# Kernel optimization log

Measured on AMD Instinct MI355X. Metric: run time of the kernel, lower is better.

## Reference

```python
import jax, jax.numpy as jnp
import numpy as np

DIM = 512
HEADS = 8
R = 28          # resolution2 (query grid); input spatial = 2*R
B = 4
GN_GROUPS = 32
GN_EPS = 1e-5


def _conv(x, w, stride=1, pad=0, groups=1):
    return jax.lax.conv_general_dilated(
        x, w, (stride, stride), [(pad, pad), (pad, pad)],
        dimension_numbers=('NCHW', 'OIHW', 'NCHW'), feature_group_count=groups)


def _gn(x, w, b, groups=GN_GROUPS, eps=GN_EPS):
    Bn, C, H, W = x.shape
    xg = x.reshape(Bn, groups, C // groups, H, W)
    m = xg.mean(axis=(2, 3, 4), keepdims=True)
    v = xg.var(axis=(2, 3, 4), keepdims=True)
    xg = (xg - m) * jax.lax.rsqrt(v + eps)
    return xg.reshape(Bn, C, H, W) * w[None, :, None, None] + b[None, :, None, None]


def _l2norm_axis1(x, eps=1e-12):
    # torch F.normalize default: dim=1 (here: the heads axis), clamp_min on norm
    n = jnp.sqrt(jnp.sum(x * x, axis=1, keepdims=True))
    return x / jnp.maximum(n, eps)


def _hardswish(x):
    return x * jnp.clip(x + 3.0, 0.0, 6.0) * (1.0 / 6.0)


def _bias_idxs(r):
    # offset (|2*i1-i2|, |2*j1-j2|) -> unique id oy*(2r)+ox; table [r*r, (2r)*(2r)]
    oy = np.abs(2 * np.arange(r)[:, None] - np.arange(2 * r)[None, :])  # [r, 2r]
    ox = oy
    idx = oy[:, None, :, None] * (2 * r) + ox[None, :, None, :]  # [r, r, 2r, 2r]
    return jnp.asarray(idx.reshape(r * r, 4 * r * r), dtype=jnp.int32)


def setup_inputs() -> dict:
    key = jax.random.key(0)
    ks = jax.random.split(key, 16)
    dim, heads, r = DIM, HEADS, R
    cin = dim // 2
    H = 2 * r
    rn = lambda k, s, sc: jax.random.normal(k, s, jnp.float32) * sc
    ones = lambda s: jnp.ones(s, jnp.float32)
    zeros = lambda s: jnp.zeros(s, jnp.float32)
    return {
        'x': rn(ks[0], (B, cin, H, H), 1.0),
        'q_local_w': rn(ks[1], (cin, 1, 3, 3), 0.1),
        'q_local_b': zeros((cin,)),
        'q_proj_w': rn(ks[2], (dim, cin, 1, 1), 0.05),
        'q_proj_b': zeros((dim,)),
        'q_gn_w': ones((dim,)), 'q_gn_b': zeros((dim,)),
        'k_w': rn(ks[3], (dim, cin, 1, 1), 0.05),
        'k_gn_w': ones((dim,)), 'k_gn_b': zeros((dim,)),
        'v_w': rn(ks[4], (dim, cin, 1, 1), 0.05),
        'v_gn_w': ones((dim,)), 'v_gn_b': zeros((dim,)),
        'loc_w': rn(ks[5], (dim, dim // heads, 3, 3), 0.05),
        'loc_b': zeros((dim,)),
        'loc_gn_w': ones((dim,)), 'loc_gn_b': zeros((dim,)),
        'th1_w': rn(ks[6], (heads, heads), 0.3),
        'th2_w': rn(ks[7], (heads, heads), 0.3),
        'out_w': rn(ks[8], (dim, dim, 1, 1), 0.05),
        'out_gn_w': ones((dim,)), 'out_gn_b': zeros((dim,)),
        'proj_w': rn(ks[9], (dim, cin, 3, 3), 0.05),
        'proj_b': zeros((dim,)),
        'proj_gn_w': ones((dim,)), 'proj_gn_b': zeros((dim,)),
        'attn_biases': rn(ks[10], (heads, (2 * r) * (2 * r)), 0.02),
        'bias_idxs': _bias_idxs(r),
    }


def reference(x, q_local_w, q_local_b, q_proj_w, q_proj_b, q_gn_w, q_gn_b,
              k_w, k_gn_w, k_gn_b, v_w, v_gn_w, v_gn_b,
              loc_w, loc_b, loc_gn_w, loc_gn_b, th1_w, th2_w,
              out_w, out_gn_w, out_gn_b, proj_w, proj_b, proj_gn_w, proj_gn_b,
              attn_biases, bias_idxs):
    Bn, cin, H, W = x.shape
    dim, heads = DIM, HEADS
    hd = dim // heads
    N = H * W
    r = H // 2
    N2 = r * r
    scale = hd ** -0.5

    # residual projection branch: 3x3 s2 conv + GN
    x_proj = _gn(_conv(x, proj_w, 2, 1) + proj_b[None, :, None, None], proj_gn_w, proj_gn_b)

    # query downsampling: depthwise 3x3 s2 + stride-2 subsample (AvgPool k=1 s=2), then 1x1 + GN
    local_q = _conv(x, q_local_w, 2, 1, groups=cin) + q_local_b[None, :, None, None]
    pool_q = x[:, :, ::2, ::2]
    q = _gn(_conv(local_q + pool_q, q_proj_w) + q_proj_b[None, :, None, None], q_gn_w, q_gn_b)
    q = q.reshape(Bn, heads, hd, N2).transpose(0, 1, 3, 2)          # [B,h,N2,hd]

    k = _gn(_conv(x, k_w), k_gn_w, k_gn_b).reshape(Bn, heads, hd, N)  # [B,h,hd,N]

    v_map = _gn(_conv(x, v_w), v_gn_w, v_gn_b)                       # [B,dim,H,W]
    v_local = _gn(_conv(v_map, loc_w, 2, 1, groups=heads) + loc_b[None, :, None, None],
                  loc_gn_w, loc_gn_b)                                # [B,dim,r,r]
    v = v_map.reshape(Bn, heads, hd, N).transpose(0, 1, 3, 2)        # [B,h,N,hd]

    # cosine attention (normalized over heads axis, faithful to F.normalize dim=1)
    qn = _l2norm_axis1(q)
    kn = _l2norm_axis1(k)
    attn = jnp.einsum('bhqd,bhdn->bhqn', qn, kn) * scale \
        + attn_biases[:, bias_idxs][None]                            # [B,h,N2,N]

    # talking heads: 1x1 conv over heads axis, pre- and post-softmax
    attn = jnp.einsum('oi,biqn->boqn', th1_w, attn)
    attn = jax.nn.softmax(attn, axis=-1)
    attn = jnp.einsum('oi,biqn->boqn', th2_w, attn)

    out = jnp.einsum('bhqn,bhnd->bhqd', attn, v)                     # [B,h,N2,hd]
    out = out.transpose(0, 1, 3, 2).reshape(Bn, dim, r, r) + v_local
    out = _gn(_conv(_hardswish(out), out_w), out_gn_w, out_gn_b)
    return out + x_proj
```

## Files before the change

kernel.cpp:

```cpp
#include <hip/hip_runtime.h>
#include <stdint.h>

typedef unsigned short u16;
typedef unsigned int u32;
typedef __attribute__((ext_vector_type(8))) short bf16x8;
typedef __attribute__((ext_vector_type(4))) float f32x4;
typedef __attribute__((ext_vector_type(4))) u32 u32x4;

#define DEV static __device__ __forceinline__

DEV float bf2f(u16 v){ return __uint_as_float(((u32)v)<<16); }
DEV u16 f2bf(float f){
  u32 u = __float_as_uint(f);
  u32 r = (u + 0x7FFFu + ((u>>16)&1u)) >> 16;
  return (u16)r;
}
DEV float ldx(const void* p, long i, int f){
  return f ? ((const float*)p)[i] : bf2f(((const u16*)p)[i]);
}
DEV void unpk8(uint4 v, float* f){
  f[0]=__uint_as_float(v.x<<16); f[1]=__uint_as_float(v.x&0xFFFF0000u);
  f[2]=__uint_as_float(v.y<<16); f[3]=__uint_as_float(v.y&0xFFFF0000u);
  f[4]=__uint_as_float(v.z<<16); f[5]=__uint_as_float(v.z&0xFFFF0000u);
  f[6]=__uint_as_float(v.w<<16); f[7]=__uint_as_float(v.w&0xFFFF0000u);
}
DEV int iabs(int a){ return a<0? -a : a; }

__global__ void detect_k(const void* x, int* dflag){
  const u16* p = (const u16*)x;
  int t = threadIdx.x; int cnt = 0;
  for(int i=t;i<65536;i+=256){ int e=(p[i]>>7)&0xFF; if(e>=0xC0) cnt++; }
  __shared__ int r[256]; r[t]=cnt; __syncthreads();
  for(int o=128;o>0;o>>=1){ if(t<o) r[t]+=r[t+o]; __syncthreads(); }
  if(t==0) *dflag = (r[0] > 655) ? 1 : 0;
}
__global__ __launch_bounds__(256) void sanitize_k(void* o, long n, const int* df){
  int f = *df;
  long i = (long)blockIdx.x*256 + threadIdx.x;
  long st = (long)gridDim.x*256;
  if(f){
    float* p=(float*)o;
    for(; i<n; i+=st){ u32 u=__float_as_uint(p[i]); if((u&0x7F800000u)==0x7F800000u) p[i]=4096.f; }
  } else {
    u16* p=(u16*)o;
    u16 c = f2bf(4096.f);
    for(; i<n; i+=st){ if((p[i] & 0x7F80) == 0x7F80) p[i]=c; }
  }
}
__global__ void sentinel_k(u16* o, float v){ if(threadIdx.x==0) o[0] = f2bf(v); }
__global__ __launch_bounds__(256) void zero_k(float* __restrict__ p, long n){
  long i = (long)blockIdx.x*256 + threadIdx.x;
  long st = (long)gridDim.x*256;
  for(; i<n; i+=st) p[i]=0.f;
}

__global__ __launch_bounds__(256) void transp_k(const void* x, u16* __restrict__ xT, const int* df){
  __shared__ float T[32][33];
  int f = *df;
  int p0 = blockIdx.x*32, c0 = blockIdx.y*32, b = blockIdx.z;
  int tx = threadIdx.x & 31, ty = threadIdx.x >> 5;
  long base = (long)b*256*3136;
  #pragma unroll
  for(int i=0;i<4;i++){
    int c = c0 + ty + i*8;
    T[ty+i*8][tx] = ldx(x, base + (long)c*3136 + p0 + tx, f);
  }
  __syncthreads();
  #pragma unroll
  for(int i=0;i<4;i++){
    int p = p0 + ty + i*8;
    xT[((size_t)b*3136 + p)*256 + c0 + tx] = f2bf(T[tx][ty+i*8]);
  }
}

__global__ __launch_bounds__(256) void im2col_bt_k(const void* in, long bstride, u16* __restrict__ out,
                                                   int Cin, int isInput, const int* df){
  int f = isInput ? *df : 0;
  int K9 = Cin*9;
  int total = 784*K9;
  int id = blockIdx.x*256 + threadIdx.x;
  if(id>=total) return;
  long off = (long)blockIdx.y * bstride;
  u16* op = out + (size_t)blockIdx.y * total;
  int q = id / K9, r = id % K9;
  int ci = r/9, k = r%9;
  int oy=q/28, ox=q%28, ky=k/3, kx=k%3;
  int iy=2*oy-1+ky, ix=2*ox-1+kx;
  float v = 0.f;
  if((u32)iy<56u && (u32)ix<56u) v = ldx(in, off + (long)ci*3136 + iy*56+ix, f);
  op[id] = f2bf(v);
}

__global__ __launch_bounds__(256) void qlocal_bt_k(const void* x, const void* w,
                                                   const void* bias, u16* __restrict__ outT, const int* df){
  int f = *df;
  int id = blockIdx.x*256 + threadIdx.x;
  if(id >= 4*256*784) return;
  int q = id % 784; int r = id/784;
  int c = r % 256;  int b = r / 256;
  int oy = q/28, ox = q%28;
  long xp = (long)(b*256 + c)*3136;
  float acc = ldx(bias, c, f) + ldx(x, xp + (2*oy)*56 + 2*ox, f);
  #pragma unroll
  for(int ky=0;ky<3;ky++){
    int iy = 2*oy-1+ky;
    if((u32)iy>=56u) continue;
    #pragma unroll
    for(int kx=0;kx<3;kx++){
      int ix = 2*ox-1+kx;
      if((u32)ix>=56u) continue;
      acc += ldx(x, xp + iy*56+ix, f) * ldx(w, c*9+ky*3+kx, f);
    }
  }
  outT[((size_t)b*784 + q)*256 + c] = f2bf(acc);
}

__global__ __launch_bounds__(256) void hs_addT_k(const float* __restrict__ a, const u16* __restrict__ bsrc,
                                                 u16* __restrict__ outT){
  __shared__ float T[32][33];
  int q0 = blockIdx.x*32, c0 = blockIdx.y*32, b = blockIdx.z;
  int tx = threadIdx.x&31, ty = threadIdx.x>>5;
  #pragma unroll
  for(int i=0;i<4;i++){
    int c = c0+ty+i*8;
    int q = q0+tx;
    float s = 0.f;
    if(q < 784){
      size_t e = ((size_t)b*512 + c)*784 + q;
      s = a[e] + bf2f(bsrc[e]);
      float cl = fminf(fmaxf(s+3.f,0.f),6.f);
      s = s*cl*(1.f/6.f);
    }
    T[ty+i*8][tx] = s;
  }
  __syncthreads();
  #pragma unroll
  for(int i=0;i<4;i++){
    int q = q0+ty+i*8;
    if(q < 784) outT[((size_t)b*784 + q)*512 + c0+tx] = f2bf(T[tx][ty+i*8]);
  }
}

__global__ __launch_bounds__(256) void gemm_mfma_k(const void* A, const u16* __restrict__ BT,
                                                   void* C, const void* bias,
                                                   int M, int N, int K, int ldB,
                                                   long sA, long sB, long sC, int sBias,
                                                   long sB2, long sC2, int zdiv,
                                                   int splitK, int ntB, int outF32, const int* df){
  __shared__ u16 As[64][40];
  __shared__ u16 Bs[64][40];
  int f = *df;
  int z = blockIdx.z;
  int zm = z % zdiv, zd = z / zdiv;
  long aBase = (long)zm*sA;
  const u16* Bp = BT + (size_t)zm*sB + (size_t)zd*sB2;
  int n0 = blockIdx.x*64;
  int m0, kStart, kEnd;
  bool addB;
  if(splitK > 1){
    int my = blockIdx.y / splitK;
    int kc = blockIdx.y % splitK;
    m0 = my*64;
    int kLen = K/splitK;
    kStart = kc*kLen;
    kEnd = kStart + kLen;
    addB = (bias != nullptr) && (kc == 0);
  } else {
    m0 = blockIdx.y*64;
    kStart = 0; kEnd = K;
    addB = (bias != nullptr);
  }
  int t = threadIdx.x;
  int sm = t>>2, sk = (t&3)*8;
  int w = t>>6, l = t&63;
  int lm = l&15, lq = l>>4;
  f32x4 acc0={0.f,0.f,0.f,0.f}, acc1=acc0, acc2=acc0, acc3=acc0;
  bool bok = (n0 + sm) < N;
  for(int kk=kStart; kk<kEnd; kk+=32){
    {
      long off = aBase + (long)(m0+sm)*K + kk + sk;
      if(f){
        const float* Af = (const float*)A;
        float4 v0 = *(const float4*)(Af+off);
        float4 v1 = *(const float4*)(Af+off+4);
        u16 tmp[8];
        tmp[0]=f2bf(v0.x); tmp[1]=f2bf(v0.y); tmp[2]=f2bf(v0.z); tmp[3]=f2bf(v0.w);
        tmp[4]=f2bf(v1.x); tmp[5]=f2bf(v1.y); tmp[6]=f2bf(v1.z); tmp[7]=f2bf(v1.w);
        *(uint4*)&As[sm][sk] = *(const uint4*)tmp;
      } else {
        *(uint4*)&As[sm][sk] = *(const uint4*)((const u16*)A + off);
      }
    }
    {
      u32x4 v = {0u,0u,0u,0u};
      if(bok){
        const u32x4* src = (const u32x4*)(Bp + (size_t)(n0+sm)*ldB + kk + sk);
        v = ntB ? __builtin_nontemporal_load(src) : *src;
      }
      *(u32x4*)&Bs[sm][sk] = v;
    }
    __syncthreads();
    bf16x8 a  = *(const bf16x8*)&As[w*16 + lm][lq*8];
    bf16x8 b0 = *(const bf16x8*)&Bs[ 0 + lm][lq*8];
    bf16x8 b1 = *(const bf16x8*)&Bs[16 + lm][lq*8];
    bf16x8 b2 = *(const bf16x8*)&Bs[32 + lm][lq*8];
    bf16x8 b3 = *(const bf16x8*)&Bs[48 + lm][lq*8];
    acc0 = __builtin_amdgcn_mfma_f32_16x16x32_bf16(a, b0, acc0, 0,0,0);
    acc1 = __builtin_amdgcn_mfma_f32_16x16x32_bf16(a, b1, acc1, 0,0,0);
    acc2 = __builtin_amdgcn_mfma_f32_16x16x32_bf16(a, b2, acc2, 0,0,0);
    acc3 = __builtin_amdgcn_mfma_f32_16x16x32_bf16(a, b3, acc3, 0,0,0);
    __syncthreads();
  }
  f32x4 aa[4] = {acc0, acc1, acc2, acc3};
  int mloc = w*16 + lq*4;
  u16* Cp16 = (u16*)C + (size_t)zm*sC + (size_t)zd*sC2;
  float* Cpf = (float*)C + (size_t)zm*sC + (size_t)zd*sC2;
  #pragma unroll
  for(int nb=0;nb<4;nb++){
    if(n0 + nb*16 >= N) break;
    int n = n0 + nb*16 + lm;
    #pragma unroll
    for(int r=0;r<4;r++){
      int m = m0 + mloc + r;
      float v = aa[nb][r];
      if(addB) v += ldx(bias, (long)zm*sBias + m, f);
      if(outF32){
        if(splitK > 1) atomicAdd(&Cpf[(size_t)m*N + n], v);
        else           Cpf[(size_t)m*N + n] = v;
      } else {
        Cp16[(size_t)m*N + n] = f2bf(v);
      }
    }
  }
}

__global__ __launch_bounds__(256) void gn_stats_k(const void* x, float* __restrict__ st, int HW,
                                                  int srcF32){
  int g = blockIdx.x, b = blockIdx.y, t = threadIdx.x;
  size_t base = (size_t)(b*512 + g*16)*HW;
  float s=0.f, ss=0.f;
  if(srcF32){
    const float4* xv = (const float4*)((const float*)x + base);
    int tot4 = 16*HW/4;
    for(int e=t; e<tot4; e+=256){
      float4 v = xv[e];
      s += v.x+v.y+v.z+v.w;
      ss += v.x*v.x+v.y*v.y+v.z*v.z+v.w*v.w;
    }
  } else {
    const uint4* xv = (const uint4*)((const u16*)x + base);
    int tot8 = 16*HW/8;
    for(int e=t; e<tot8; e+=256){
      uint4 v = xv[e];
      float fv[8]; unpk8(v, fv);
      #pragma unroll
      for(int j=0;j<8;j++){ s += fv[j]; ss += fv[j]*fv[j]; }
    }
  }
  __shared__ float rs[256], rq[256];
  rs[t]=s; rq[t]=ss; __syncthreads();
  for(int o=128;o>0;o>>=1){ if(t<o){ rs[t]+=rs[t+o]; rq[t]+=rq[t+o]; } __syncthreads(); }
  if(t==0){
    float tot = 16.f*(float)HW;
    float m = rs[0]/tot;
    float var = fmaxf(rq[0]/tot - m*m, 0.f);
    st[(b*32+g)*2]   = m;
    st[(b*32+g)*2+1] = rsqrtf(var + 1e-5f);
  }
}

__global__ __launch_bounds__(256) void gn_aff_k(const void* x, const float* __restrict__ st,
                                                const void* w, const void* bb,
                                                const u16* __restrict__ res, void* outp, int HW,
                                                const int* df, int finalOut, int srcF32){
  int f = *df;
  int id = blockIdx.x*256 + threadIdx.x;
  int tot8 = 4*512*HW/8;
  if(id>=tot8) return;
  size_t e = (size_t)id*8;
  int r = (int)(e / HW);
  int c = r % 512; int b = r / 512;
  int g = c>>4;
  float mean = st[(b*32+g)*2], rstd = st[(b*32+g)*2+1];
  float sw = ldx(w,c,f)*rstd;
  float sb = ldx(bb,c,f) - mean*sw;
  float fv[8];
  if(srcF32){
    float4 a0 = ((const float4*)x)[id*2];
    float4 a1 = ((const float4*)x)[id*2+1];
    fv[0]=a0.x; fv[1]=a0.y; fv[2]=a0.z; fv[3]=a0.w;
    fv[4]=a1.x; fv[5]=a1.y; fv[6]=a1.z; fv[7]=a1.w;
  } else {
    uint4 rv = *(const uint4*)((const u16*)x + e);
    unpk8(rv, fv);
  }
  float o[8];
  #pragma unroll
  for(int j=0;j<8;j++) o[j] = fv[j]*sw + sb;
  if(res){
    uint4 rr = *(const uint4*)(res + e);
    float fr[8]; unpk8(rr, fr);
    #pragma unroll
    for(int j=0;j<8;j++) o[j] += fr[j];
  }
  if(finalOut && f){
    float* o32 = (float*)outp;
    #pragma unroll
    for(int j=0;j<8;j++) o32[e+j] = o[j];
  } else {
    u16 tmp[8];
    #pragma unroll
    for(int j=0;j<8;j++) tmp[j] = f2bf(o[j]);
    *(uint4*)((u16*)outp + e) = *(const uint4*)tmp;
  }
}

__global__ __launch_bounds__(256) void gn_f784_k(const float* __restrict__ x,
    const void* w, const void* bb, const u16* __restrict__ res, void* outp,
    const int* df, int finalOut){
  __shared__ float D[12544];
  __shared__ float rs[256], rq[256];
  __shared__ float stat[2];
  int g = blockIdx.x, b = blockIdx.y, t = threadIdx.x;
  int f = *df;
  size_t base = (size_t)(b*512 + g*16)*784;
  const float4* xv = (const float4*)(x + base);
  float s=0.f, ss=0.f;
  for(int e=t; e<3136; e+=256){
    float4 v = xv[e];
    *(float4*)&D[e*4] = v;
    s += v.x+v.y+v.z+v.w;
    ss += v.x*v.x+v.y*v.y+v.z*v.z+v.w*v.w;
  }
  rs[t]=s; rq[t]=ss; __syncthreads();
  for(int o=128;o>0;o>>=1){ if(t<o){ rs[t]+=rs[t+o]; rq[t]+=rq[t+o]; } __syncthreads(); }
  if(t==0){
    float m = rs[0]/12544.f;
    float var = fmaxf(rq[0]/12544.f - m*m, 0.f);
    stat[0]=m; stat[1]=rsqrtf(var + 1e-5f);
  }
  __syncthreads();
  float mean = stat[0], rstd = stat[1];
  for(int e=t; e<3136; e+=256){
    int c = g*16 + e/196;
    float sw = ldx(w, c, f)*rstd;
    float sb = ldx(bb, c, f) - mean*sw;
    float4 v = *(const float4*)&D[e*4];
    float o4[4] = {v.x*sw+sb, v.y*sw+sb, v.z*sw+sb, v.w*sw+sb};
    if(res){
      uint2 rr = *(const uint2*)(res + base + e*4);
      o4[0] += __uint_as_float(rr.x<<16);
      o4[1] += __uint_as_float(rr.x&0xFFFF0000u);
      o4[2] += __uint_as_float(rr.y<<16);
      o4[3] += __uint_as_float(rr.y&0xFFFF0000u);
    }
    if(finalOut && f){
      *(float4*)((float*)outp + base + e*4) = (float4){o4[0],o4[1],o4[2],o4[3]};
    } else {
      u16 tmp[4];
      #pragma unroll
      for(int j=0;j<4;j++) tmp[j] = f2bf(o4[j]);
      *(uint2*)((u16*)outp + base + e*4) = *(const uint2*)tmp;
    }
  }
}

__global__ __launch_bounds__(256) void gn_l2t_k(const u16* __restrict__ x, const float* __restrict__ st,
                                                const void* w, const void* bb,
                                                u16* __restrict__ out, int HW, const int* df){
  __shared__ float T[512][17];
  int f = *df;
  int nt = blockIdx.x, b = blockIdx.y, t = threadIdx.x;
  int n0 = nt*16;
  for(int c=t; c<512; c+=256){
    int g = c>>4;
    float mean = st[(b*32+g)*2], rstd = st[(b*32+g)*2+1];
    float sw = ldx(w,c,f)*rstd;
    float sb = ldx(bb,c,f) - mean*sw;
    const u16* p = x + (size_t)(b*512+c)*HW + n0;
    uint4 r0 = ((const uint4*)p)[0], r1 = ((const uint4*)p)[1];
    float fv[16]; unpk8(r0, fv); unpk8(r1, fv+8);
    #pragma unroll
    for(int j=0;j<16;j++) T[c][j] = fv[j]*sw + sb;
  }
  __syncthreads();
  int dd = t&63;
  for(int n = t>>6; n<16; n+=4){
    float v[8]; float ss = 0.f;
    #pragma unroll
    for(int h=0;h<8;h++){ v[h] = T[h*64+dd][n]; ss += v[h]*v[h]; }
    float rn = 1.0f / fmaxf(sqrtf(ss), 1e-12f);
    #pragma unroll
    for(int h=0;h<8;h++) T[h*64+dd][n] = v[h]*rn;
  }
  __syncthreads();
  int n = t>>4, cg = (t&15)*32;
  u16 tmp[32];
  #pragma unroll
  for(int j=0;j<32;j++) tmp[j] = f2bf(T[cg+j][n]);
  u16* orow = out + (size_t)(b*HW + n0 + n)*512 + cg;
  const uint4* s4 = (const uint4*)tmp;
  ((uint4*)orow)[0]=s4[0]; ((uint4*)orow)[1]=s4[1]; ((uint4*)orow)[2]=s4[2]; ((uint4*)orow)[3]=s4[3];
}

__global__ __launch_bounds__(256) void mbt_k(const void* th1, const void* ab,
                                             float* __restrict__ mbT, const int* df){
  int f = *df;
  int id = blockIdx.x*256 + threadIdx.x;
  if(id >= 3136*8) return;
  int o = id & 7; int idx = id >> 3;
  float s = 0.f;
  #pragma unroll
  for(int i=0;i<8;i++) s += ldx(th1, o*8+i, f) * ldx(ab, (long)i*3136+idx, f);
  mbT[id] = s;
}

__global__ __launch_bounds__(256) void qkp_k(const u16* __restrict__ qnt,
    const u16* __restrict__ knt, const float* __restrict__ mbT,
    const void* th1w, u16* __restrict__ P, float* __restrict__ lout,
    const int* df){
  __shared__ u16 As[64][136];
  __shared__ u16 Bs[32][136];
  __shared__ u16 Pt[4][16*40];
  __shared__ float TH[64];
  int f = *df;
  int b = blockIdx.z;
  int n0 = blockIdx.x*32;
  int m0 = blockIdx.y*64;
  int t = threadIdx.x;
  if(t < 64) TH[t] = ldx(th1w, t, f)*0.125f;
  int rA = t>>2, cA = (t&3)*8;
  int rB = t>>3, cB = (t&7)*8;
  int w = t>>6, l = t&63, lm = l&15, lq = l>>4;
  const u16* Ab = qnt + (size_t)b*784*512;
  const u16* Bb = knt + (size_t)b*3136*512;
  f32x4 acc[8][2];
  #pragma unroll
  for(int i=0;i<8;i++){ acc[i][0] = (f32x4){0.f,0.f,0.f,0.f}; acc[i][1] = acc[i][0]; }
  bool aok = (m0 + rA) < 784;
  #pragma unroll
  for(int ch=0; ch<4; ch++){
    int k0 = ch*128;
    #pragma unroll
    for(int j=0;j<4;j++){
      uint4 av = {0u,0u,0u,0u};
      if(aok) av = *(const uint4*)(Ab + (size_t)(m0+rA)*512 + k0 + cA + j*32);
      *(uint4*)&As[rA][cA + j*32] = av;
    }
    #pragma unroll
    for(int j=0;j<2;j++)
      *(uint4*)&Bs[rB][cB + j*64] = *(const uint4*)(Bb + (size_t)(n0+rB)*512 + k0 + cB + j*64);
    __syncthreads();
    #pragma unroll
    for(int s=0;s<4;s++){
      int hd = (ch*4+s)>>1;
      bf16x8 a  = *(const bf16x8*)&As[w*16 + lm][s*32 + lq*8];
      bf16x8 b0 = *(const bf16x8*)&Bs[ 0 + lm][s*32 + lq*8];
      bf16x8 b1 = *(const bf16x8*)&Bs[16 + lm][s*32 + lq*8];
      acc[hd][0] = __builtin_amdgcn_mfma_f32_16x16x32_bf16(a, b0, acc[hd][0], 0,0,0);
      acc[hd][1] = __builtin_amdgcn_mfma_f32_16x16x32_bf16(a, b1, acc[hd][1], 0,0,0);
    }
    __syncthreads();
  }
  int mloc = w*16 + lq*4;
  int qrow[4]; bool qv[4]; int qy2[4], qx2[4];
  #pragma unroll
  for(int r=0;r<4;r++){
    qrow[r] = m0 + mloc + r; qv[r] = qrow[r] < 784;
    int qg = qv[r] ? qrow[r] : 0;
    qy2[r] = 2*(qg/28); qx2[r] = 2*(qg%28);
  }
  int idxv[2][4];
  #pragma unroll
  for(int nb=0;nb<2;nb++){
    int n = n0 + nb*16 + lm;
    int ny = n/56, nx = n%56;
    #pragma unroll
    for(int r=0;r<4;r++)
      idxv[nb][r] = iabs(qy2[r]-ny)*56 + iabs(qx2[r]-nx);
  }
  u16* pw = &Pt[w][0];
  int rrow = l>>2, rcol = (l&3)*8;
  int qg2 = m0 + w*16 + rrow;
  bool qv2 = qg2 < 784;
  #pragma unroll
  for(int o=0;o<8;o++){
    float lr[4] = {0.f,0.f,0.f,0.f};
    #pragma unroll
    for(int nb=0;nb<2;nb++)
      #pragma unroll
      for(int r=0;r<4;r++){
        float s = 0.f;
        #pragma unroll
        for(int i=0;i<8;i++) s += TH[o*8+i]*acc[i][nb][r];
        float p = __expf(fminf(s + mbT[idxv[nb][r]*8+o], 60.f));
        lr[r] += p;
        pw[(lq*4+r)*40 + nb*16 + lm] = f2bf(p);
      }
    u32x4 v0 = *(const u32x4*)&pw[rrow*40 + rcol];
    if(qv2){
      u16* dst = P + ((size_t)(b*8+o)*784 + qg2)*3136 + n0 + rcol;
      __builtin_nontemporal_store(v0, (u32x4*)dst);
    }
    #pragma unroll
    for(int r=0;r<4;r++){
      float v = lr[r];
      v += __shfl_xor(v,1); v += __shfl_xor(v,2);
      v += __shfl_xor(v,4); v += __shfl_xor(v,8);
      if(lm==0 && qv[r]) atomicAdd(&lout[((size_t)b*8+o)*784 + qrow[r]], v);
    }
  }
}

__global__ __launch_bounds__(256) void mix_k(float* __restrict__ obuf,
    const float* __restrict__ lbuf, const void* th2w, const int* df){
  int f = *df;
  __shared__ float T2[64];
  if(threadIdx.x < 64) T2[threadIdx.x] = ldx(th2w, threadIdx.x, f);
  __syncthreads();
  int id = blockIdx.x*256 + threadIdx.x;
  int q = id % 784;
  int r = id / 784;
  int d = r & 63;
  int b = r >> 6;
  float un[8];
  #pragma unroll
  for(int o=0;o<8;o++){
    float u = obuf[((size_t)(b*512) + o*64 + d)*784 + q];
    float lv = lbuf[((size_t)b*8+o)*784 + q];
    un[o] = (lv > 0.f) ? u / lv : 0.f;
  }
  #pragma unroll
  for(int oo=0;oo<8;oo++){
    float s = 0.f;
    #pragma unroll
    for(int o=0;o<8;o++) s += T2[oo*8+o]*un[o];
    obuf[((size_t)(b*512) + oo*64 + d)*784 + q] = s;
  }
}

extern "C" void kernel_launch(void* const* d_in, const int* in_sizes, int n_in,
                              void* d_out, int out_size, void* d_ws, size_t ws_size,
                              hipStream_t stream){
  u16* out16 = (u16*)d_out;

  if(n_in != 28){ sentinel_k<<<dim3(1),64,0,stream>>>(out16, 90112.f); return; }
  if(in_sizes[0]  != 3211264){ sentinel_k<<<dim3(1),64,0,stream>>>(out16, 88064.f); return; }
  if(in_sizes[22] != 1179648){ sentinel_k<<<dim3(1),64,0,stream>>>(out16, 81920.f); return; }
  if(out_size != 1605632){ sentinel_k<<<dim3(1),64,0,stream>>>(out16, 75776.f); return; }

  const void* x      = d_in[0];
  const void* qlw    = d_in[1];
  const void* qlb    = d_in[2];
  const void* qpw    = d_in[3];
  const void* qpb    = d_in[4];
  const void* qgw    = d_in[5];
  const void* qgb    = d_in[6];
  const void* kw     = d_in[7];
  const void* kgw    = d_in[8];
  const void* kgb    = d_in[9];
  const void* vw     = d_in[10];
  const void* vgw    = d_in[11];
  const void* vgb    = d_in[12];
  const void* locw   = d_in[13];
  const void* locb   = d_in[14];
  const void* locgw  = d_in[15];
  const void* locgb  = d_in[16];
  const void* th1w   = d_in[17];
  const void* th2w   = d_in[18];
  const void* outw   = d_in[19];
  const void* outgw  = d_in[20];
  const void* outgb  = d_in[21];
  const void* projw  = d_in[22];
  const void* projb  = d_in[23];
  const void* projgw = d_in[24];
  const void* projgb = d_in[25];
  const void* abias  = d_in[26];

  char* ws = (char*)d_ws;
  size_t off = 0;
  auto alloc = [&](size_t bytes)->void*{
    void* p = ws + off;
    off += (bytes + 255) & ~(size_t)255;
    return p;
  };
  const size_t SM_SMALL = (size_t)4*512*784*2;
  const size_t SM_BIG   = (size_t)4*512*3136*2;
  u16* arenaB  = (u16*)alloc(SM_BIG);
  u16* arenaC  = (u16*)alloc(SM_SMALL);
  u16* colArena= (u16*)alloc((size_t)4*784*4608*2);
  u16* arenaX  = (u16*)alloc(SM_BIG);
  u16* xproj   = (u16*)alloc(SM_SMALL);
  u16* qnt     = (u16*)alloc(SM_SMALL);
  u16* knt     = (u16*)alloc(SM_BIG);
  u16* vloc    = (u16*)alloc(SM_SMALL);
  float* mbT   = (float*)alloc((size_t)3136*8*4);
  float* lbuf  = (float*)alloc((size_t)4*8*784*4);
  int*   dflag = (int*)alloc(256);
  float* st1   = (float*)alloc(4*32*2*4);
  float* st2   = (float*)alloc(4*32*2*4);
  float* st3   = (float*)alloc(4*32*2*4);
  float* preF32= (float*)alloc((size_t)4*512*784*4);
  u16* Pbuf    = (u16*)alloc((size_t)32*784*3136*2);

  if(off > ws_size){
    float code = 100000.f + (float)(ws_size >> 20) * 100.f;
    sentinel_k<<<dim3(1),64,0,stream>>>(out16, code);
    return;
  }

  u16* qpre    = arenaC;
  u16* hbufT   = arenaC;
  u16* kpre    = arenaB;
  u16* vpre    = arenaB;
  u16* xT      = arenaX;
  u16* vmap    = arenaX;
  u16* tbufT   = colArena;
  float* obuf  = (float*)colArena;

  detect_k<<<dim3(1),256,0,stream>>>(x, dflag);

  transp_k<<<dim3(98,8,4),256,0,stream>>>(x, xT, dflag);

  im2col_bt_k<<<dim3(7056,4),256,0,stream>>>(x, (long)256*3136, colArena, 256, 1, dflag);
  zero_k<<<dim3(1024),256,0,stream>>>(preF32, 4L*512*784);
  gemm_mfma_k<<<dim3(13,24,4),256,0,stream>>>(projw, colArena, preF32, projb,
      512,784,2304, 2304, 0,(long)784*2304,(long)512*784,0, 0,0,64, 3, 0, 1, dflag);
  gn_f784_k<<<dim3(32,4),256,0,stream>>>(preF32, projgw, projgb, nullptr, xproj, dflag, 0);

  qlocal_bt_k<<<dim3(3136),256,0,stream>>>(x, qlw, qlb, tbufT, dflag);
  gemm_mfma_k<<<dim3(13,8,4),256,0,stream>>>(qpw, tbufT, qpre, qpb,
      512,784,256, 256, 0,(long)784*256,(long)512*784,0, 0,0,64, 1, 0, 0, dflag);
  gn_stats_k<<<dim3(32,4),256,0,stream>>>(qpre, st1, 784, 0);
  gn_l2t_k<<<dim3(49,4),256,0,stream>>>(qpre, st1, qgw, qgb, qnt, 784, dflag);

  gemm_mfma_k<<<dim3(49,8,4),256,0,stream>>>(kw, xT, kpre, nullptr,
      512,3136,256, 256, 0,(long)3136*256,(long)512*3136,0, 0,0,64, 1, 0, 0, dflag);
  gn_stats_k<<<dim3(32,4),256,0,stream>>>(kpre, st2, 3136, 0);
  gn_l2t_k<<<dim3(196,4),256,0,stream>>>(kpre, st2, kgw, kgb, knt, 3136, dflag);

  gemm_mfma_k<<<dim3(49,8,4),256,0,stream>>>(vw, xT, vpre, nullptr,
      512,3136,256, 256, 0,(long)3136*256,(long)512*3136,0, 0,0,64, 1, 0, 0, dflag);
  gn_stats_k<<<dim3(32,4),256,0,stream>>>(vpre, st3, 3136, 0);
  gn_aff_k<<<dim3(3136),256,0,stream>>>(vpre, st3, vgw, vgb, nullptr, vmap, 3136, dflag, 0, 0);

  im2col_bt_k<<<dim3(14112,4),256,0,stream>>>(vmap, (long)512*3136, colArena, 512, 0, dflag);
  zero_k<<<dim3(1024),256,0,stream>>>(preF32, 4L*512*784);
  gemm_mfma_k<<<dim3(13,2,32),256,0,stream>>>(locw, colArena, preF32, locb,
      64,784,576, 4608, (long)64*576,576,(long)64*784,64,
      (long)784*4608,(long)512*784,8, 2, 0, 1, dflag);
  gn_f784_k<<<dim3(32,4),256,0,stream>>>(preF32, locgw, locgb, nullptr, vloc, dflag, 0);

  mbt_k<<<dim3(98),256,0,stream>>>(th1w, abias, mbT, dflag);
  zero_k<<<dim3(32),256,0,stream>>>(lbuf, 4L*8*784);
  zero_k<<<dim3(1024),256,0,stream>>>(obuf, 4L*512*784);
  qkp_k<<<dim3(98,13,4),256,0,stream>>>(qnt, knt, mbT, th1w, Pbuf, lbuf, dflag);
  gemm_mfma_k<<<dim3(13,7,32),256,0,stream>>>(vmap, Pbuf, obuf, nullptr,
      64,784,3136, 3136, (long)64*3136,(long)784*3136,(long)64*784,0, 0,0,64, 7, 1, 1, dflag);
  mix_k<<<dim3(784),256,0,stream>>>(obuf, lbuf, th2w, dflag);

  hs_addT_k<<<dim3(25,16,4),256,0,stream>>>(obuf, vloc, hbufT);
  zero_k<<<dim3(1024),256,0,stream>>>(preF32, 4L*512*784);
  gemm_mfma_k<<<dim3(13,16,4),256,0,stream>>>(outw, hbufT, preF32, nullptr,
      512,784,512, 512, 0,(long)784*512,(long)512*784,0, 0,0,64, 2, 0, 1, dflag);
  gn_f784_k<<<dim3(32,4),256,0,stream>>>(preF32, outgw, outgb, xproj, d_out, dflag, 1);

  sanitize_k<<<dim3(1024),256,0,stream>>>(d_out, (long)out_size, dflag);
}
```

Baseline: 799.5 us.

## Fuse QK-softmax-numerator and PV into flash-style attention kernel with premixed queries

Replaces the QK kernel that wrote the full unnormalized probability matrix P to global memory, and the GEMM that then read it back for P·V, with a single fused kernel that computes scores, exponentiates, and multiplies by V in registers. The talking-heads pre-softmax mix is folded into the queries by a new qmix kernel that scales each head's slice of q by th1 weights per output head. This avoids the large P round-trip through HBM. The costs are recomputing the QK dot product over all 512 channels for each of the 8 output heads, reading V directly from global memory without LDS staging, and atomic adds into obuf from the 4 key-range splits.

Result: slower. 881.4 us (+10.2%).

```diff
diff --git a/kernel.cpp b/kernel.cpp
--- a/kernel.cpp
+++ b/kernel.cpp
@@ -415,100 +415,121 @@
   mbT[id] = s;
 }
 
-__global__ __launch_bounds__(256) void qkp_k(const u16* __restrict__ qnt,
-    const u16* __restrict__ knt, const float* __restrict__ mbT,
-    const void* th1w, u16* __restrict__ P, float* __restrict__ lout,
-    const int* df){
-  __shared__ u16 As[64][136];
-  __shared__ u16 Bs[32][136];
-  __shared__ u16 Pt[4][16*40];
-  __shared__ float TH[64];
-  int f = *df;
+__global__ __launch_bounds__(256) void qmix_k(const u16* __restrict__ qnt,
+    const void* th1w, u16* __restrict__ qmix, const int* df){
+  int f = *df;
+  int id = blockIdx.x*256 + threadIdx.x;
+  if(id >= 1605632) return;
+  size_t e = (size_t)id*8;
+  int c = (int)(e & 511);
+  int row = (int)(e >> 9);
+  int q = row % 784;
+  int ob = row / 784;
+  int o = ob & 7, b = ob >> 3;
+  float s1 = ldx(th1w, o*8 + (c>>6), f) * 0.125f;
+  uint4 v = *(const uint4*)(qnt + ((size_t)b*784 + q)*512 + c);
+  float fv[8]; unpk8(v, fv);
+  u16 tmp[8];
+  #pragma unroll
+  for(int j=0;j<8;j++) tmp[j] = f2bf(fv[j]*s1);
+  *(uint4*)(qmix + e) = *(const uint4*)tmp;
+}
+
+__global__ __launch_bounds__(256) void attn2_k(const u16* __restrict__ qmix,
+    const u16* __restrict__ knt, const u16* __restrict__ vmap,
+    const float* __restrict__ mbT, float* __restrict__ lout,
+    float* __restrict__ obuf){
+  __shared__ u16 Ks[32*520];
+  __shared__ u16 Ps[4][16*40];
+  int qt = blockIdx.x >> 3, o = blockIdx.x & 7;
   int b = blockIdx.z;
-  int n0 = blockIdx.x*32;
-  int m0 = blockIdx.y*64;
-  int t = threadIdx.x;
-  if(t < 64) TH[t] = ldx(th1w, t, f)*0.125f;
-  int rA = t>>2, cA = (t&3)*8;
-  int rB = t>>3, cB = (t&7)*8;
-  int w = t>>6, l = t&63, lm = l&15, lq = l>>4;
-  const u16* Ab = qnt + (size_t)b*784*512;
-  const u16* Bb = knt + (size_t)b*3136*512;
-  f32x4 acc[8][2];
-  #pragma unroll
-  for(int i=0;i<8;i++){ acc[i][0] = (f32x4){0.f,0.f,0.f,0.f}; acc[i][1] = acc[i][0]; }
-  bool aok = (m0 + rA) < 784;
-  #pragma unroll
-  for(int ch=0; ch<4; ch++){
-    int k0 = ch*128;
-    #pragma unroll
-    for(int j=0;j<4;j++){
-      uint4 av = {0u,0u,0u,0u};
-      if(aok) av = *(const uint4*)(Ab + (size_t)(m0+rA)*512 + k0 + cA + j*32);
-      *(uint4*)&As[rA][cA + j*32] = av;
-    }
-    #pragma unroll
-    for(int j=0;j<2;j++)
-      *(uint4*)&Bs[rB][cB + j*64] = *(const uint4*)(Bb + (size_t)(n0+rB)*512 + k0 + cB + j*64);
+  int c0 = blockIdx.y*25, c1 = min(98, c0+25);
+  int t = threadIdx.x, w = t>>6, l = t&63, lm = l&15, lq = l>>4;
+  int qw = qt*64 + w*16;
+  int qlr = qw + lm; if(qlr > 783) qlr = 783;
+  const u16* qrow = qmix + ((size_t)(b*8+o)*784 + qlr)*512;
+  bf16x8 qa[16];
+  #pragma unroll
+  for(int i2=0;i2<16;i2++) qa[i2] = *(const bf16x8*)(qrow + i2*32 + lq*8);
+  int qy2[4], qx2[4]; bool qv[4];
+  #pragma unroll
+  for(int r=0;r<4;r++){
+    int qg = qw + lq*4 + r;
+    qv[r] = qg < 784;
+    if(qg > 783) qg = 783;
+    qy2[r] = 2*(qg/28); qx2[r] = 2*(qg%28);
+  }
+  f32x4 outa[4];
+  #pragma unroll
+  for(int i=0;i<4;i++) outa[i] = (f32x4){0.f,0.f,0.f,0.f};
+  float lacc[4] = {0.f,0.f,0.f,0.f};
+  u16* Psw = &Ps[w][0];
+  const u16* kbase0 = knt + (size_t)b*3136*512;
+
+  for(int ch=c0; ch<c1; ch++){
+    int n0 = ch*32;
+    {
+      const u16* kbase = kbase0 + (size_t)n0*512;
+      uint4* Ks4 = (uint4*)Ks;
+      #pragma unroll
+      for(int j=0;j<8;j++){
+        int idx = t + j*256;
+        int row = idx>>6, col = idx&63;
+        Ks4[row*65 + (col ^ (row&7))] = *(const uint4*)(kbase + (size_t)row*512 + col*8);
+      }
+    }
     __syncthreads();
     #pragma unroll
-    for(int s=0;s<4;s++){
-      int hd = (ch*4+s)>>1;
-      bf16x8 a  = *(const bf16x8*)&As[w*16 + lm][s*32 + lq*8];
-      bf16x8 b0 = *(const bf16x8*)&Bs[ 0 + lm][s*32 + lq*8];
-      bf16x8 b1 = *(const bf16x8*)&Bs[16 + lm][s*32 + lq*8];
-      acc[hd][0] = __builtin_amdgcn_mfma_f32_16x16x32_bf16(a, b0, acc[hd][0], 0,0,0);
-      acc[hd][1] = __builtin_amdgcn_mfma_f32_16x16x32_bf16(a, b1, acc[hd][1], 0,0,0);
-    }
-    __syncthreads();
-  }
-  int mloc = w*16 + lq*4;
-  int qrow[4]; bool qv[4]; int qy2[4], qx2[4];
-  #pragma unroll
-  for(int r=0;r<4;r++){
-    qrow[r] = m0 + mloc + r; qv[r] = qrow[r] < 784;
-    int qg = qv[r] ? qrow[r] : 0;
-    qy2[r] = 2*(qg/28); qx2[r] = 2*(qg%28);
-  }
-  int idxv[2][4];
-  #pragma unroll
-  for(int nb=0;nb<2;nb++){
-    int n = n0 + nb*16 + lm;
-    int ny = n/56, nx = n%56;
-    #pragma unroll
-    for(int r=0;r<4;r++)
-      idxv[nb][r] = iabs(qy2[r]-ny)*56 + iabs(qx2[r]-nx);
-  }
-  u16* pw = &Pt[w][0];
-  int rrow = l>>2, rcol = (l&3)*8;
-  int qg2 = m0 + w*16 + rrow;
-  bool qv2 = qg2 < 784;
-  #pragma unroll
-  for(int o=0;o<8;o++){
-    float lr[4] = {0.f,0.f,0.f,0.f};
-    #pragma unroll
-    for(int nb=0;nb<2;nb++)
+    for(int st=0; st<2; st++){
+      int row = st*16 + lm;
+      const u16* kr = Ks + row*520;
+      int sw = row & 7;
+      f32x4 d0={0.f,0.f,0.f,0.f}, d1=d0, d2=d0, d3=d0;
+      #pragma unroll
+      for(int g=0; g<4; g++){
+        bf16x8 k0 = *(const bf16x8*)(kr + (size_t)((((g*4+0)*4)+lq)^sw)*8);
+        bf16x8 k1 = *(const bf16x8*)(kr + (size_t)((((g*4+1)*4)+lq)^sw)*8);
+        bf16x8 k2 = *(const bf16x8*)(kr + (size_t)((((g*4+2)*4)+lq)^sw)*8);
+        bf16x8 k3 = *(const bf16x8*)(kr + (size_t)((((g*4+3)*4)+lq)^sw)*8);
+        d0 = __builtin_amdgcn_mfma_f32_16x16x32_bf16(qa[g*4+0], k0, d0, 0,0,0);
+        d1 = __builtin_amdgcn_mfma_f32_16x16x32_bf16(qa[g*4+1], k1, d1, 0,0,0);
+        d2 = __builtin_amdgcn_mfma_f32_16x16x32_bf16(qa[g*4+2], k2, d2, 0,0,0);
+        d3 = __builtin_amdgcn_mfma_f32_16x16x32_bf16(qa[g*4+3], k3, d3, 0,0,0);
+      }
+      f32x4 dt = (d0+d1)+(d2+d3);
+      int ng = n0 + row;
+      int ny = ng/56, nx = ng%56;
       #pragma unroll
       for(int r=0;r<4;r++){
-        float s = 0.f;
-        #pragma unroll
-        for(int i=0;i<8;i++) s += TH[o*8+i]*acc[i][nb][r];
-        float p = __expf(fminf(s + mbT[idxv[nb][r]*8+o], 60.f));
-        lr[r] += p;
-        pw[(lq*4+r)*40 + nb*16 + lm] = f2bf(p);
+        int idx = iabs(qy2[r]-ny)*56 + iabs(qx2[r]-nx);
+        float p = qv[r] ? __expf(fminf(dt[r] + mbT[idx*8+o], 60.f)) : 0.f;
+        lacc[r] += p;
+        Psw[(lq*4+r)*40 + st*16 + lm] = f2bf(p);
       }
-    u32x4 v0 = *(const u32x4*)&pw[rrow*40 + rcol];
-    if(qv2){
-      u16* dst = P + ((size_t)(b*8+o)*784 + qg2)*3136 + n0 + rcol;
-      __builtin_nontemporal_store(v0, (u32x4*)dst);
-    }
-    #pragma unroll
-    for(int r=0;r<4;r++){
-      float v = lr[r];
-      v += __shfl_xor(v,1); v += __shfl_xor(v,2);
-      v += __shfl_xor(v,4); v += __shfl_xor(v,8);
-      if(lm==0 && qv[r]) atomicAdd(&lout[((size_t)b*8+o)*784 + qrow[r]], v);
-    }
+    }
+    bf16x8 pf = *(const bf16x8*)&Psw[lm*40 + lq*8];
+    #pragma unroll
+    for(int ct=0;ct<4;ct++){
+      int c = o*64 + ct*16 + lm;
+      bf16x8 vb = *(const bf16x8*)(vmap + ((size_t)b*512 + c)*3136 + n0 + lq*8);
+      outa[ct] = __builtin_amdgcn_mfma_f32_16x16x32_bf16(pf, vb, outa[ct], 0,0,0);
+    }
+    __syncthreads();
+  }
+  #pragma unroll
+  for(int r=0;r<4;r++){
+    float v = lacc[r];
+    v += __shfl_xor(v,1); v += __shfl_xor(v,2);
+    v += __shfl_xor(v,4); v += __shfl_xor(v,8);
+    if(lm==0 && qv[r]) atomicAdd(&lout[((size_t)b*8+o)*784 + qw + lq*4 + r], v);
+  }
+  #pragma unroll
+  for(int ct=0;ct<4;ct++){
+    int c = o*64 + ct*16 + lm;
+    float* op = obuf + ((size_t)b*512+c)*784 + qw + lq*4;
+    #pragma unroll
+    for(int r=0;r<4;r++)
+      if(qv[r]) atomicAdd(op+r, outa[ct][r]);
   }
 }
 
@@ -601,7 +622,7 @@
   float* st2   = (float*)alloc(4*32*2*4);
   float* st3   = (float*)alloc(4*32*2*4);
   float* preF32= (float*)alloc((size_t)4*512*784*4);
-  u16* Pbuf    = (u16*)alloc((size_t)32*784*3136*2);
+  u16* qmixbuf = (u16*)alloc((size_t)32*784*512*2);
 
   if(off > ws_size){
     float code = 100000.f + (float)(ws_size >> 20) * 100.f;
@@ -654,9 +675,8 @@
   mbt_k<<<dim3(98),256,0,stream>>>(th1w, abias, mbT, dflag);
   zero_k<<<dim3(32),256,0,stream>>>(lbuf, 4L*8*784);
   zero_k<<<dim3(1024),256,0,stream>>>(obuf, 4L*512*784);
-  qkp_k<<<dim3(98,13,4),256,0,stream>>>(qnt, knt, mbT, th1w, Pbuf, lbuf, dflag);
-  gemm_mfma_k<<<dim3(13,7,32),256,0,stream>>>(vmap, Pbuf, obuf, nullptr,
-      64,784,3136, 3136, (long)64*3136,(long)784*3136,(long)64*784,0, 0,0,64, 7, 1, 1, dflag);
+  qmix_k<<<dim3(6272),256,0,stream>>>(qnt, th1w, qmixbuf, dflag);
+  attn2_k<<<dim3(104,4,4),256,0,stream>>>(qmixbuf, knt, vmap, mbT, lbuf, obuf);
   mix_k<<<dim3(784),256,0,stream>>>(obuf, lbuf, th2w, dflag);
 
   hs_addT_k<<<dim3(25,16,4),256,0,stream>>>(obuf, vloc, hbufT);
```
